# Kernel tuning notes

Measured on AMD Instinct MI355X. Metric: run time of the kernel, lower is better.

## Reference

```python
import jax, jax.numpy as jnp
import numpy as np
from jax import lax

B, T, D, A = 32, 2048, 1024, 1024

def setup_inputs() -> dict:
    key = jax.random.key(0)
    ks = jax.random.split(key, 8)
    s = 1.0 / np.sqrt(D)
    return {
        "query": jax.random.normal(ks[0], (B, 1, D), jnp.float32),
        "value": jax.random.normal(ks[1], (B, T, D), jnp.float32),
        "last_attn": jax.random.uniform(ks[2], (B, T), jnp.float32),
        "conv_w": jax.random.normal(ks[3], (A, 1, 3), jnp.float32) * 0.1,
        "conv_b": jnp.zeros((A,), jnp.float32),
        "Wq": jax.random.normal(ks[4], (A, D), jnp.float32) * s,
        "Wv": jax.random.normal(ks[5], (A, D), jnp.float32) * s,
        "bias": jax.random.uniform(ks[6], (A,), jnp.float32, -0.1, 0.1),
        "fc_w": jax.random.normal(ks[7], (1, A), jnp.float32) * (1.0 / np.sqrt(A)),
        "fc_b": jnp.zeros((1,), jnp.float32),
    }

def reference(query, value, last_attn, conv_w, conv_b, Wq, Wv, bias, fc_w, fc_b):
    # location conv1d: (B,1,T) -> (B,A,T), kernel 3, pad 1
    loc = lax.conv_general_dilated(
        last_attn[:, None, :], conv_w, window_strides=(1,), padding="SAME",
        dimension_numbers=("NCH", "OIH", "NCH"))
    loc = loc + conv_b[None, :, None]
    loc = jnp.transpose(loc, (0, 2, 1))  # (B, T, A)
    # fused add + bias + tanh; query proj (B,1,A) broadcasts over T
    hidden = jnp.tanh(query @ Wq.T + value @ Wv.T + loc + bias)  # (B, T, A)
    energy = (hidden @ fc_w.T + fc_b)[..., 0]  # (B, T)
    attn = jax.nn.softmax(energy, axis=-1)  # (B, T)
    context = jnp.einsum("bt,btd->bd", attn, value)[:, None, :]  # (B, 1, D)
    return context, attn
```

## Files before the change

### kernel.cpp

```cpp
#include <hip/hip_runtime.h>
#include <stdint.h>

#define AS1 __attribute__((address_space(1)))
#define AS3 __attribute__((address_space(3)))

typedef __bf16 bf16x8 __attribute__((ext_vector_type(8)));
typedef float  f32x4  __attribute__((ext_vector_type(4)));

__global__ __launch_bounds__(256) void prep_all(
    const float* __restrict__ value, __bf16* __restrict__ vbf,
    const float* __restrict__ Wv,    __bf16* __restrict__ wvbf,
    const float* __restrict__ q,     const float* __restrict__ Wq,
    const float* __restrict__ bias,  const float* __restrict__ convb,
    float* __restrict__ qb2,         float* __restrict__ ctx)
{
    const int bid = blockIdx.x, tid = threadIdx.x;
    if (bid < 32768) {
        int i = bid * 256 + tid;
        const float4* p = (const float4*)value + (size_t)i * 2;
        float4 x = p[0], y = p[1];
        bf16x8 v;
        v[0] = (__bf16)x.x; v[1] = (__bf16)x.y; v[2] = (__bf16)x.z; v[3] = (__bf16)x.w;
        v[4] = (__bf16)y.x; v[5] = (__bf16)y.y; v[6] = (__bf16)y.z; v[7] = (__bf16)y.w;
        *((bf16x8*)vbf + i) = v;
    } else if (bid < 33280) {
        int i = (bid - 32768) * 256 + tid;
        const float4* p = (const float4*)Wv + (size_t)i * 2;
        float4 x = p[0], y = p[1];
        bf16x8 v;
        v[0] = (__bf16)x.x; v[1] = (__bf16)x.y; v[2] = (__bf16)x.z; v[3] = (__bf16)x.w;
        v[4] = (__bf16)y.x; v[5] = (__bf16)y.y; v[6] = (__bf16)y.z; v[7] = (__bf16)y.w;
        *((bf16x8*)wvbf + i) = v;
        if (i < 4096) {
            float4 z = {0.f, 0.f, 0.f, 0.f};
            ((float4*)ctx)[i * 2]     = z;
            ((float4*)ctx)[i * 2 + 1] = z;
        }
    } else {
        int wid  = tid >> 6;
        int lane = tid & 63;
        int a    = (bid - 33280) * 4 + wid;
        const float* wr_ = Wq + (size_t)a * 1024;
        float w[16];
#pragma unroll
        for (int j = 0; j < 16; ++j) w[j] = wr_[lane + 64 * j];
        float bb = bias[a] + convb[a];
        for (int b = 0; b < 32; ++b) {
            const float* qr = q + (size_t)b * 1024;
            float s = 0.f;
#pragma unroll
            for (int j = 0; j < 16; ++j) s += w[j] * qr[lane + 64 * j];
            for (int m = 1; m < 64; m <<= 1) s += __shfl_xor(s, m);
            if (lane == 0) qb2[b * 1024 + a] = s + bb;
        }
    }
}

__global__ __launch_bounds__(256, 4) void gemm_fused(
    const __bf16* __restrict__ Abf,
    const __bf16* __restrict__ Bbf,
    const float*  __restrict__ qb2,
    const float*  __restrict__ la,
    const float*  __restrict__ convw,
    const float*  __restrict__ fcw,
    float* __restrict__ ep)
{
    constexpr int K = 1024, NT = 16;
    __shared__ __bf16 As[128 * 64];
    __shared__ __bf16 Bs[128 * 64];

    const int tid  = threadIdx.x;
    const int lane = tid & 63;
    const int wid  = tid >> 6;
    const int wr   = wid >> 1, wc = wid & 1;

    const int bid = blockIdx.x;
    const int swz = (bid & 7) * 512 + (bid >> 3);
    const int rt  = swz >> 3;
    const int ct  = swz & 7;
    const int rowBase = rt * 128;
    const int colBase = ct * 128;

    f32x4 acc[4][4] = {};

#pragma unroll 1
    for (int t = 0; t < NT; ++t) {
        const int k0 = t * 64;
#pragma unroll
        for (int is = 0; is < 4; ++is) {
            int idx16 = is * 256 + tid;
            int r     = idx16 >> 3;
            int ssw   = (idx16 ^ r) & 7;
            const __bf16* ga = Abf + (size_t)(rowBase + r) * K + k0 + ssw * 8;
            __builtin_amdgcn_global_load_lds((AS1 void*)ga, (AS3 void*)(&As[idx16 * 8]), 16, 0, 0);
            const __bf16* gb = Bbf + (size_t)(colBase + r) * K + k0 + ssw * 8;
            __builtin_amdgcn_global_load_lds((AS1 void*)gb, (AS3 void*)(&Bs[idx16 * 8]), 16, 0, 0);
        }
        __syncthreads();
#pragma unroll
        for (int kk = 0; kk < 2; ++kk) {
            bf16x8 af[4], bfr[4];
#pragma unroll
            for (int mi = 0; mi < 4; ++mi) {
                int row  = wr * 64 + mi * 16 + (lane & 15);
                int slot = (kk * 4 + (lane >> 4)) ^ (row & 7);
                af[mi] = *(const bf16x8*)(&As[row * 64 + slot * 8]);
            }
#pragma unroll
            for (int ni = 0; ni < 4; ++ni) {
                int row  = wc * 64 + ni * 16 + (lane & 15);
                int slot = (kk * 4 + (lane >> 4)) ^ (row & 7);
                bfr[ni] = *(const bf16x8*)(&Bs[row * 64 + slot * 8]);
            }
#pragma unroll
            for (int mi = 0; mi < 4; ++mi)
#pragma unroll
                for (int ni = 0; ni < 4; ++ni)
                    acc[mi][ni] = __builtin_amdgcn_mfma_f32_16x16x32_bf16(
                        af[mi], bfr[ni], acc[mi][ni], 0, 0, 0);
        }
        __syncthreads();
    }

    const int b     = rowBase >> 11;
    const int tTile = rowBase & 2047;
    const float* lab  = la  + (size_t)b * 2048;
    const float* qrow = qb2 + (size_t)b * 1024;

    float cw0[4], cw1[4], cw2[4], fv[4], qv[4];
#pragma unroll
    for (int ni = 0; ni < 4; ++ni) {
        int a = colBase + wc * 64 + ni * 16 + (lane & 15);
        cw0[ni] = convw[a * 3 + 0];
        cw1[ni] = convw[a * 3 + 1];
        cw2[ni] = convw[a * 3 + 2];
        fv[ni]  = fcw[a];
        qv[ni]  = qrow[a];
    }
    float* eps = (float*)&As[0];
    const int g4 = (lane >> 4) * 4;
#pragma unroll
    for (int mi = 0; mi < 4; ++mi) {
#pragma unroll
        for (int j = 0; j < 4; ++j) {
            int rloc = wr * 64 + mi * 16 + g4 + j;
            int t = tTile + rloc;
            float p1 = lab[t];
            float p0 = (t > 0)    ? lab[t - 1] : 0.f;
            float p2 = (t < 2047) ? lab[t + 1] : 0.f;
            float sum = 0.f;
#pragma unroll
            for (int ni = 0; ni < 4; ++ni) {
                float e = acc[mi][ni][j] + qv[ni] + cw0[ni] * p0 + cw1[ni] * p1 + cw2[ni] * p2;
                float h = 1.f - 2.f / (1.f + __expf(2.f * e));
                sum += fv[ni] * h;
            }
            sum += __shfl_xor(sum, 1);
            sum += __shfl_xor(sum, 2);
            sum += __shfl_xor(sum, 4);
            sum += __shfl_xor(sum, 8);
            if ((lane & 15) == 0)
                eps[rloc * 2 + wc] = sum;
        }
    }
    __syncthreads();
    if (tid < 128) {
        float e = eps[tid * 2 + 0] + eps[tid * 2 + 1];
        ep[(size_t)ct * 65536 + rowBase + tid] = e;
    }
}

__global__ __launch_bounds__(256) void context_softmax(const float* __restrict__ ep,
                                                       const __bf16* __restrict__ vbf,
                                                       float* __restrict__ attn,
                                                       float* __restrict__ ctx) {
    int b = blockIdx.x, tc = blockIdx.y, tid = threadIdx.x;
    __shared__ float e[2048];
    __shared__ float red[4], red2[4];

    float e8[8];
    float m = -1e30f;
#pragma unroll
    for (int k = 0; k < 8; ++k) {
        int t = tid + 256 * k;
        float s = 0.f;
#pragma unroll
        for (int ct = 0; ct < 8; ++ct) s += ep[(size_t)ct * 65536 + b * 2048 + t];
        e8[k] = s;
        m = fmaxf(m, s);
    }
    for (int s = 1; s < 64; s <<= 1) m = fmaxf(m, __shfl_xor(m, s));
    if ((tid & 63) == 0) red[tid >> 6] = m;
    __syncthreads();
    m = fmaxf(fmaxf(red[0], red[1]), fmaxf(red[2], red[3]));

    float s = 0.f, vals[8];
#pragma unroll
    for (int k = 0; k < 8; ++k) {
        vals[k] = __expf(e8[k] - m);
        s += vals[k];
        e[tid + 256 * k] = vals[k];
    }
    for (int t2 = 1; t2 < 64; t2 <<= 1) s += __shfl_xor(s, t2);
    if ((tid & 63) == 0) red2[tid >> 6] = s;
    __syncthreads();
    s = red2[0] + red2[1] + red2[2] + red2[3];
    float inv = 1.f / s;

    if (tc == 0) {
#pragma unroll
        for (int k = 0; k < 8; ++k)
            attn[(size_t)b * 2048 + tid + 256 * k] = vals[k] * inv;
    }

    int half = tid >> 7, dc = tid & 127;
    int t0 = tc * 256 + half * 128;
    const float*  wv_ = &e[t0];
    const __bf16* vb  = vbf + ((size_t)(b * 2048 + t0)) * 1024 + dc * 8;
    float c[8] = {};
#pragma unroll 4
    for (int t = 0; t < 128; ++t) {
        float  w = wv_[t] * inv;
        bf16x8 v = *(const bf16x8*)(vb + (size_t)t * 1024);
#pragma unroll
        for (int k = 0; k < 8; ++k) c[k] += w * (float)v[k];
    }
    float* out = ctx + (size_t)b * 1024 + dc * 8;
#pragma unroll
    for (int k = 0; k < 8; ++k) atomicAdd(out + k, c[k]);
}

extern "C" void kernel_launch(void* const* d_in, const int* in_sizes, int n_in,
                              void* d_out, int out_size, void* d_ws, size_t ws_size,
                              hipStream_t stream) {
    const float* query     = (const float*)d_in[0];
    const float* value     = (const float*)d_in[1];
    const float* last_attn = (const float*)d_in[2];
    const float* conv_w    = (const float*)d_in[3];
    const float* conv_b    = (const float*)d_in[4];
    const float* Wq        = (const float*)d_in[5];
    const float* Wv        = (const float*)d_in[6];
    const float* bias      = (const float*)d_in[7];
    const float* fc_w      = (const float*)d_in[8];

    float* ctx  = (float*)d_out;
    float* attn = (float*)d_out + 32 * 1024;

    const size_t VBF_B  = (size_t)65536 * 1024 * 2;
    const size_t WVBF_B = (size_t)1024 * 1024 * 2;
    const size_t QB2_B  = (size_t)32 * 1024 * 4;
    const size_t EP_B   = (size_t)8 * 32 * 2048 * 4;
    if (ws_size < VBF_B + WVBF_B + QB2_B + EP_B) return;

    char*   ws   = (char*)d_ws;
    __bf16* vbf  = (__bf16*)ws;
    __bf16* wvbf = (__bf16*)(ws + VBF_B);
    float*  qb2  = (float*)(ws + VBF_B + WVBF_B);
    float*  ep   = (float*)(ws + VBF_B + WVBF_B + QB2_B);

    prep_all<<<33536, 256, 0, stream>>>(value, vbf, Wv, wvbf,
                                        query, Wq, bias, conv_b, qb2, ctx);

    gemm_fused<<<4096, 256, 0, stream>>>(vbf, wvbf, qb2, last_attn, conv_w, fc_w, ep);

    dim3 gc(32, 8);
    context_softmax<<<gc, 256, 0, stream>>>(ep, vbf, attn, ctx);
}
```

Baseline: 296.6 us.

## Double-buffer GEMM LDS tiles with K=32 stages to overlap loads and MFMA

Replaces the single-buffered 64-wide K tile with two 32-wide LDS buffers. The next tile's global_load_lds is issued before computing the current one, which leaves one barrier per iteration. LDS addresses are precomputed with a new pair-row swizzle. The aim is to hide global-load latency behind MFMA work. In exchange there are twice as many iterations, and correctness relies on how global_load_lds completion is ordered against the barrier.

```diff
diff --git a/kernel.cpp b/kernel.cpp
--- a/kernel.cpp
+++ b/kernel.cpp
@@ -65,9 +65,9 @@
     const float*  __restrict__ fcw,
     float* __restrict__ ep)
 {
-    constexpr int K = 1024, NT = 16;
-    __shared__ __bf16 As[128 * 64];
-    __shared__ __bf16 Bs[128 * 64];
+    constexpr int K = 1024, NT = 32;
+    __shared__ __bf16 As[2][128 * 32];
+    __shared__ __bf16 Bs[2][128 * 32];
 
     const int tid  = threadIdx.x;
     const int lane = tid & 63;
@@ -83,44 +83,59 @@
 
     f32x4 acc[4][4] = {};
 
+    const int c0 = tid, c1 = tid + 256;
+    const int R0 = c0 >> 3, R1 = c1 >> 3;
+    const int r0 = R0 * 2 + ((c0 >> 2) & 1), s0 = (c0 & 3) ^ (R0 & 3);
+    const int r1 = R1 * 2 + ((c1 >> 2) & 1), s1 = (c1 & 3) ^ (R1 & 3);
+    const __bf16* pa0 = Abf + (size_t)(rowBase + r0) * K + s0 * 8;
+    const __bf16* pa1 = Abf + (size_t)(rowBase + r1) * K + s1 * 8;
+    const __bf16* pb0 = Bbf + (size_t)(colBase + r0) * K + s0 * 8;
+    const __bf16* pb1 = Bbf + (size_t)(colBase + r1) * K + s1 * 8;
+
+    auto STAGE = [&](int buf, int k0) {
+        __builtin_amdgcn_global_load_lds((AS1 void*)(pa0 + k0), (AS3 void*)(&As[buf][c0 * 8]), 16, 0, 0);
+        __builtin_amdgcn_global_load_lds((AS1 void*)(pa1 + k0), (AS3 void*)(&As[buf][c1 * 8]), 16, 0, 0);
+        __builtin_amdgcn_global_load_lds((AS1 void*)(pb0 + k0), (AS3 void*)(&Bs[buf][c0 * 8]), 16, 0, 0);
+        __builtin_amdgcn_global_load_lds((AS1 void*)(pb1 + k0), (AS3 void*)(&Bs[buf][c1 * 8]), 16, 0, 0);
+    };
+
+    int offA[4], offB[4];
+    {
+        const int s = lane >> 4;
+#pragma unroll
+        for (int i = 0; i < 4; ++i) {
+            int rowA = wr * 64 + i * 16 + (lane & 15);
+            int RA = rowA >> 1;
+            offA[i] = RA * 64 + (rowA & 1) * 32 + ((s ^ (RA & 3)) * 8);
+            int rowB = wc * 64 + i * 16 + (lane & 15);
+            int RB = rowB >> 1;
+            offB[i] = RB * 64 + (rowB & 1) * 32 + ((s ^ (RB & 3)) * 8);
+        }
+    }
+
+    auto COMPUTE = [&](int buf) {
+        bf16x8 af[4], bfr[4];
+#pragma unroll
+        for (int i = 0; i < 4; ++i) af[i]  = *(const bf16x8*)(&As[buf][offA[i]]);
+#pragma unroll
+        for (int i = 0; i < 4; ++i) bfr[i] = *(const bf16x8*)(&Bs[buf][offB[i]]);
+#pragma unroll
+        for (int mi = 0; mi < 4; ++mi)
+#pragma unroll
+            for (int ni = 0; ni < 4; ++ni)
+                acc[mi][ni] = __builtin_amdgcn_mfma_f32_16x16x32_bf16(
+                    af[mi], bfr[ni], acc[mi][ni], 0, 0, 0);
+    };
+
+    STAGE(0, 0);
+    __syncthreads();
 #pragma unroll 1
-    for (int t = 0; t < NT; ++t) {
-        const int k0 = t * 64;
-#pragma unroll
-        for (int is = 0; is < 4; ++is) {
-            int idx16 = is * 256 + tid;
-            int r     = idx16 >> 3;
-            int ssw   = (idx16 ^ r) & 7;
-            const __bf16* ga = Abf + (size_t)(rowBase + r) * K + k0 + ssw * 8;
-            __builtin_amdgcn_global_load_lds((AS1 void*)ga, (AS3 void*)(&As[idx16 * 8]), 16, 0, 0);
-            const __bf16* gb = Bbf + (size_t)(colBase + r) * K + k0 + ssw * 8;
-            __builtin_amdgcn_global_load_lds((AS1 void*)gb, (AS3 void*)(&Bs[idx16 * 8]), 16, 0, 0);
-        }
+    for (int t = 0; t < NT - 1; ++t) {
+        STAGE((t + 1) & 1, (t + 1) * 32);
+        COMPUTE(t & 1);
         __syncthreads();
-#pragma unroll
-        for (int kk = 0; kk < 2; ++kk) {
-            bf16x8 af[4], bfr[4];
-#pragma unroll
-            for (int mi = 0; mi < 4; ++mi) {
-                int row  = wr * 64 + mi * 16 + (lane & 15);
-                int slot = (kk * 4 + (lane >> 4)) ^ (row & 7);
-                af[mi] = *(const bf16x8*)(&As[row * 64 + slot * 8]);
-            }
-#pragma unroll
-            for (int ni = 0; ni < 4; ++ni) {
-                int row  = wc * 64 + ni * 16 + (lane & 15);
-                int slot = (kk * 4 + (lane >> 4)) ^ (row & 7);
-                bfr[ni] = *(const bf16x8*)(&Bs[row * 64 + slot * 8]);
-            }
-#pragma unroll
-            for (int mi = 0; mi < 4; ++mi)
-#pragma unroll
-                for (int ni = 0; ni < 4; ++ni)
-                    acc[mi][ni] = __builtin_amdgcn_mfma_f32_16x16x32_bf16(
-                        af[mi], bfr[ni], acc[mi][ni], 0, 0, 0);
-        }
-        __syncthreads();
-    }
+    }
+    COMPUTE(1);
 
     const int b     = rowBase >> 11;
     const int tTile = rowBase & 2047;
@@ -137,7 +152,7 @@
         fv[ni]  = fcw[a];
         qv[ni]  = qrow[a];
     }
-    float* eps = (float*)&As[0];
+    float* eps = (float*)&As[0][0];
     const int g4 = (lane >> 4) * 4;
 #pragma unroll
     for (int mi = 0; mi < 4; ++mi) {
```

Measured after the change: 316.6 us. 6.7% more time.

## Use 256x256 tiles with double-buffered LDS and interleaved load/MFMA phases

Applied to the files above, without the earlier changes.

Enlarges the GEMM tile from 128x128 to 256x256 with 512 threads (8 waves) and double-buffers the LDS tiles. Each k-step is split into four quadrant phases, with async global-to-LDS loads for later steps interleaved between MFMA groups and s_setprio raised around the MFMA groups. Column tiles drop from 8 to 4, so the partial-energy buffer and the softmax reduction shrink to match. The aim is more operand reuse per byte loaded and hiding global-load latency behind MFMA work. The cost is far fewer blocks (1024), more LDS per block and heavy reliance on hand-tuned vmcnt counts and barriers being correct.

```diff
diff --git a/kernel.cpp b/kernel.cpp
--- a/kernel.cpp
+++ b/kernel.cpp
@@ -56,7 +56,7 @@
     }
 }
 
-__global__ __launch_bounds__(256, 4) void gemm_fused(
+__global__ __launch_bounds__(512, 2) void gemm_fused(
     const __bf16* __restrict__ Abf,
     const __bf16* __restrict__ Bbf,
     const float*  __restrict__ qb2,
@@ -66,62 +66,158 @@
     float* __restrict__ ep)
 {
     constexpr int K = 1024, NT = 16;
-    __shared__ __bf16 As[128 * 64];
-    __shared__ __bf16 Bs[128 * 64];
+    __shared__ __bf16 As[2][256 * 64];
+    __shared__ __bf16 Bs[2][256 * 64];
 
     const int tid  = threadIdx.x;
     const int lane = tid & 63;
     const int wid  = tid >> 6;
-    const int wr   = wid >> 1, wc = wid & 1;
+    const int wr   = wid >> 2, wc = wid & 3;
 
     const int bid = blockIdx.x;
-    const int swz = (bid & 7) * 512 + (bid >> 3);
-    const int rt  = swz >> 3;
-    const int ct  = swz & 7;
-    const int rowBase = rt * 128;
-    const int colBase = ct * 128;
-
-    f32x4 acc[4][4] = {};
+    const int swz = (bid & 7) * 128 + (bid >> 3);
+    const int rt  = swz >> 2;
+    const int ct  = swz & 3;
+    const int rowBase = rt * 256;
+    const int colBase = ct * 256;
+
+    f32x4 acc[8][4] = {};
+
+    auto STAGE_A = [&](int buf, int h, int T) {
+        const int k0 = T * 64;
+#pragma unroll
+        for (int rr = 0; rr < 2; ++rr) {
+            int idx = rr * 512 + tid;
+            int r   = idx >> 3;
+            int row = ((r >> 6) * 128) + h * 64 + (r & 63);
+            int ssw = (idx ^ r) & 7;
+            const __bf16* g = Abf + (size_t)(rowBase + row) * K + k0 + ssw * 8;
+            __builtin_amdgcn_global_load_lds((AS1 void*)g,
+                (AS3 void*)(&As[buf][row * 64 + (idx & 7) * 8]), 16, 0, 0);
+        }
+    };
+    auto STAGE_B = [&](int buf, int h, int T) {
+        const int k0 = T * 64;
+#pragma unroll
+        for (int rr = 0; rr < 2; ++rr) {
+            int idx = rr * 512 + tid;
+            int r   = idx >> 3;
+            int row = ((r >> 5) * 64) + h * 32 + (r & 31);
+            int ssw = (idx ^ r) & 7;
+            const __bf16* g = Bbf + (size_t)(colBase + row) * K + k0 + ssw * 8;
+            __builtin_amdgcn_global_load_lds((AS1 void*)g,
+                (AS3 void*)(&Bs[buf][row * 64 + (idx & 7) * 8]), 16, 0, 0);
+        }
+    };
+
+    STAGE_A(0, 0, 0); STAGE_A(0, 1, 0); STAGE_B(0, 0, 0); STAGE_B(0, 1, 0);
+    STAGE_A(1, 0, 1); STAGE_B(1, 0, 1); STAGE_B(1, 1, 1);
+    asm volatile("s_waitcnt vmcnt(6)" ::: "memory");
+    __builtin_amdgcn_s_barrier();
 
 #pragma unroll 1
-    for (int t = 0; t < NT; ++t) {
-        const int k0 = t * 64;
-#pragma unroll
-        for (int is = 0; is < 4; ++is) {
-            int idx16 = is * 256 + tid;
-            int r     = idx16 >> 3;
-            int ssw   = (idx16 ^ r) & 7;
-            const __bf16* ga = Abf + (size_t)(rowBase + r) * K + k0 + ssw * 8;
-            __builtin_amdgcn_global_load_lds((AS1 void*)ga, (AS3 void*)(&As[idx16 * 8]), 16, 0, 0);
-            const __bf16* gb = Bbf + (size_t)(colBase + r) * K + k0 + ssw * 8;
-            __builtin_amdgcn_global_load_lds((AS1 void*)gb, (AS3 void*)(&Bs[idx16 * 8]), 16, 0, 0);
-        }
-        __syncthreads();
-#pragma unroll
-        for (int kk = 0; kk < 2; ++kk) {
-            bf16x8 af[4], bfr[4];
-#pragma unroll
-            for (int mi = 0; mi < 4; ++mi) {
-                int row  = wr * 64 + mi * 16 + (lane & 15);
+    for (int T = 0; T < NT; ++T) {
+        const int buf = T & 1;
+        bf16x8 aF[4][2], bF0[2][2], bF1[2][2];
+
+        if (T + 1 == NT) {
+            asm volatile("s_waitcnt vmcnt(0)" ::: "memory");
+            __builtin_amdgcn_s_barrier();
+        } else if (T > 0) {
+            asm volatile("s_waitcnt vmcnt(6)" ::: "memory");
+            __builtin_amdgcn_s_barrier();
+        }
+
+#pragma unroll
+        for (int mi = 0; mi < 4; ++mi)
+#pragma unroll
+            for (int kk = 0; kk < 2; ++kk) {
+                int row  = wr * 128 + mi * 16 + (lane & 15);
                 int slot = (kk * 4 + (lane >> 4)) ^ (row & 7);
-                af[mi] = *(const bf16x8*)(&As[row * 64 + slot * 8]);
-            }
-#pragma unroll
-            for (int ni = 0; ni < 4; ++ni) {
+                aF[mi][kk] = *(const bf16x8*)(&As[buf][row * 64 + slot * 8]);
+            }
+#pragma unroll
+        for (int ni = 0; ni < 2; ++ni)
+#pragma unroll
+            for (int kk = 0; kk < 2; ++kk) {
                 int row  = wc * 64 + ni * 16 + (lane & 15);
                 int slot = (kk * 4 + (lane >> 4)) ^ (row & 7);
-                bfr[ni] = *(const bf16x8*)(&Bs[row * 64 + slot * 8]);
-            }
-#pragma unroll
-            for (int mi = 0; mi < 4; ++mi)
-#pragma unroll
-                for (int ni = 0; ni < 4; ++ni)
+                bF0[ni][kk] = *(const bf16x8*)(&Bs[buf][row * 64 + slot * 8]);
+            }
+        if (T < NT - 1) STAGE_A(buf ^ 1, 1, T + 1);
+        __builtin_amdgcn_s_barrier();
+        __builtin_amdgcn_s_setprio(1);
+#pragma unroll
+        for (int mi = 0; mi < 4; ++mi)
+#pragma unroll
+            for (int ni = 0; ni < 2; ++ni)
+#pragma unroll
+                for (int kk = 0; kk < 2; ++kk)
                     acc[mi][ni] = __builtin_amdgcn_mfma_f32_16x16x32_bf16(
-                        af[mi], bfr[ni], acc[mi][ni], 0, 0, 0);
-        }
-        __syncthreads();
-    }
-
+                        aF[mi][kk], bF0[ni][kk], acc[mi][ni], 0, 0, 0);
+        __builtin_amdgcn_s_setprio(0);
+        __builtin_amdgcn_s_barrier();
+
+#pragma unroll
+        for (int ni = 0; ni < 2; ++ni)
+#pragma unroll
+            for (int kk = 0; kk < 2; ++kk) {
+                int row  = wc * 64 + (2 + ni) * 16 + (lane & 15);
+                int slot = (kk * 4 + (lane >> 4)) ^ (row & 7);
+                bF1[ni][kk] = *(const bf16x8*)(&Bs[buf][row * 64 + slot * 8]);
+            }
+        if (T < NT - 2) STAGE_A(buf, 0, T + 2);
+        __builtin_amdgcn_s_barrier();
+        __builtin_amdgcn_s_setprio(1);
+#pragma unroll
+        for (int mi = 0; mi < 4; ++mi)
+#pragma unroll
+            for (int ni = 0; ni < 2; ++ni)
+#pragma unroll
+                for (int kk = 0; kk < 2; ++kk)
+                    acc[mi][2 + ni] = __builtin_amdgcn_mfma_f32_16x16x32_bf16(
+                        aF[mi][kk], bF1[ni][kk], acc[mi][2 + ni], 0, 0, 0);
+        __builtin_amdgcn_s_setprio(0);
+        __builtin_amdgcn_s_barrier();
+
+#pragma unroll
+        for (int mi = 0; mi < 4; ++mi)
+#pragma unroll
+            for (int kk = 0; kk < 2; ++kk) {
+                int row  = wr * 128 + (4 + mi) * 16 + (lane & 15);
+                int slot = (kk * 4 + (lane >> 4)) ^ (row & 7);
+                aF[mi][kk] = *(const bf16x8*)(&As[buf][row * 64 + slot * 8]);
+            }
+        if (T < NT - 2) STAGE_B(buf, 0, T + 2);
+        __builtin_amdgcn_s_barrier();
+        __builtin_amdgcn_s_setprio(1);
+#pragma unroll
+        for (int mi = 0; mi < 4; ++mi)
+#pragma unroll
+            for (int ni = 0; ni < 2; ++ni)
+#pragma unroll
+                for (int kk = 0; kk < 2; ++kk)
+                    acc[4 + mi][ni] = __builtin_amdgcn_mfma_f32_16x16x32_bf16(
+                        aF[mi][kk], bF0[ni][kk], acc[4 + mi][ni], 0, 0, 0);
+        __builtin_amdgcn_s_setprio(0);
+        __builtin_amdgcn_s_barrier();
+
+        if (T < NT - 2) STAGE_B(buf, 1, T + 2);
+        __builtin_amdgcn_s_barrier();
+        __builtin_amdgcn_s_setprio(1);
+#pragma unroll
+        for (int mi = 0; mi < 4; ++mi)
+#pragma unroll
+            for (int ni = 0; ni < 2; ++ni)
+#pragma unroll
+                for (int kk = 0; kk < 2; ++kk)
+                    acc[4 + mi][2 + ni] = __builtin_amdgcn_mfma_f32_16x16x32_bf16(
+                        aF[mi][kk], bF1[ni][kk], acc[4 + mi][2 + ni], 0, 0, 0);
+        __builtin_amdgcn_s_setprio(0);
+        __builtin_amdgcn_s_barrier();
+    }
+
+    __syncthreads();
     const int b     = rowBase >> 11;
     const int tTile = rowBase & 2047;
     const float* lab  = la  + (size_t)b * 2048;
@@ -137,13 +233,13 @@
         fv[ni]  = fcw[a];
         qv[ni]  = qrow[a];
     }
-    float* eps = (float*)&As[0];
+    float* eps = (float*)&As[0][0];
     const int g4 = (lane >> 4) * 4;
 #pragma unroll
-    for (int mi = 0; mi < 4; ++mi) {
+    for (int mi = 0; mi < 8; ++mi) {
 #pragma unroll
         for (int j = 0; j < 4; ++j) {
-            int rloc = wr * 64 + mi * 16 + g4 + j;
+            int rloc = wr * 128 + mi * 16 + g4 + j;
             int t = tTile + rloc;
             float p1 = lab[t];
             float p0 = (t > 0)    ? lab[t - 1] : 0.f;
@@ -159,13 +255,12 @@
             sum += __shfl_xor(sum, 2);
             sum += __shfl_xor(sum, 4);
             sum += __shfl_xor(sum, 8);
-            if ((lane & 15) == 0)
-                eps[rloc * 2 + wc] = sum;
+            if ((lane & 15) == 0) eps[rloc * 4 + wc] = sum;
         }
     }
     __syncthreads();
-    if (tid < 128) {
-        float e = eps[tid * 2 + 0] + eps[tid * 2 + 1];
+    if (tid < 256) {
+        float e = eps[tid * 4 + 0] + eps[tid * 4 + 1] + eps[tid * 4 + 2] + eps[tid * 4 + 3];
         ep[(size_t)ct * 65536 + rowBase + tid] = e;
     }
 }
@@ -185,7 +280,7 @@
         int t = tid + 256 * k;
         float s = 0.f;
 #pragma unroll
-        for (int ct = 0; ct < 8; ++ct) s += ep[(size_t)ct * 65536 + b * 2048 + t];
+        for (int ct = 0; ct < 4; ++ct) s += ep[(size_t)ct * 65536 + b * 2048 + t];
         e8[k] = s;
         m = fmaxf(m, s);
     }
@@ -249,7 +344,7 @@
     const size_t VBF_B  = (size_t)65536 * 1024 * 2;
     const size_t WVBF_B = (size_t)1024 * 1024 * 2;
     const size_t QB2_B  = (size_t)32 * 1024 * 4;
-    const size_t EP_B   = (size_t)8 * 32 * 2048 * 4;
+    const size_t EP_B   = (size_t)4 * 32 * 2048 * 4;
     if (ws_size < VBF_B + WVBF_B + QB2_B + EP_B) return;
 
     char*   ws   = (char*)d_ws;
@@ -261,7 +356,7 @@
     prep_all<<<33536, 256, 0, stream>>>(value, vbf, Wv, wvbf,
                                         query, Wq, bias, conv_b, qb2, ctx);
 
-    gemm_fused<<<4096, 256, 0, stream>>>(vbf, wvbf, qb2, last_attn, conv_w, fc_w, ep);
+    gemm_fused<<<1024, 512, 0, stream>>>(vbf, wvbf, qb2, last_attn, conv_w, fc_w, ep);
 
     dim3 gc(32, 8);
     context_softmax<<<gc, 256, 0, stream>>>(ep, vbf, attn, ctx);
```

Measured after the change: 306.3 us. +3.3%, slower.
